# Optimization experiments

Measured on AMD Instinct MI355X. Metric: run time of the kernel, lower is better.

The kernel has to match this reference:

```python
import jax, jax.numpy as jnp
import numpy as np

B, SQ, SC, D = 16, 1024, 1024, 768
H = 2 * D  # 1536, fc width
NCLS = 2


def setup_inputs() -> dict:
    key = jax.random.key(0)
    ks = jax.random.split(key, 8)
    q = jax.random.normal(ks[0], (B, SQ, D), jnp.float32)
    c = jax.random.normal(ks[1], (B, SC, D), jnp.float32)
    mask_q = jax.random.randint(ks[2], (B, SQ), 0, 2).astype(jnp.int32)
    mask_c = jax.random.randint(ks[3], (B, SC), 0, 2).astype(jnp.int32)
    labels = jax.random.randint(ks[4], (B,), 0, NCLS)
    # torch nn.Linear convention: weight [out, in], y = x @ W.T + b
    W1 = jax.random.normal(ks[5], (H, H), jnp.float32) * 0.02
    b1 = jnp.zeros((H,), jnp.float32)
    W2 = jax.random.normal(ks[6], (NCLS, H), jnp.float32) * 0.02
    b2 = jnp.zeros((NCLS,), jnp.float32)
    return dict(q=q, c=c, mask_q=mask_q, mask_c=mask_c, labels=labels,
                W1=W1, b1=b1, W2=W2, b2=b2)


def reference(q, c, mask_q, mask_c, labels, W1, b1, W2, b2):
    # masked QK^T score matrix: [B, SQ, SC]
    s = jnp.einsum('bik,bjk->bij', q, c)
    s = s * mask_q[:, :, None].astype(s.dtype) * mask_c[:, None, :].astype(s.dtype)
    s = jnp.where(s == 0.0, -jnp.inf, s)  # x[x == 0.0] = -inf
    p = jnp.nan_to_num(jax.nn.softmax(s, axis=2))   # softmax over context axis
    pp = jnp.nan_to_num(jax.nn.softmax(s, axis=1))  # softmax over question axis
    a = jnp.einsum('bjk,bij->bk', c, p)   # weighted combine into context feats
    bb = jnp.einsum('bik,bij->bk', q, pp)  # weighted combine into question feats
    x = jnp.concatenate([a, bb], axis=1)  # [B, 1536]
    x = jnp.tanh(x @ W1.T + b1)           # fc1 + tanh (dropout = identity in eval)
    logits = x @ W2.T + b2                # fc2
    logp = jax.nn.log_softmax(logits, axis=1)  # LogSoftmax(dim=1)
    # NLLLoss (mean reduction)
    loss = -jnp.mean(jnp.take_along_axis(logp, labels[:, None], axis=1))
    return (loss, logp)
```

## Files before the change

### kernel.cpp

```cpp
#include <hip/hip_runtime.h>
#include <math.h>

#define B_   16
#define SQ_  1024
#define SC_  1024
#define D_   768
#define H_   1536
#define BK   32
#define LDK  40

typedef __attribute__((ext_vector_type(4))) float f32x4;
typedef __attribute__((ext_vector_type(8))) short bf16x8;

__device__ __forceinline__ unsigned cvtpk(float x, float y) {
  unsigned r;
  asm("v_cvt_pk_bf16_f32 %0, %1, %2" : "=v"(r) : "v"(x), "v"(y));
  return r;
}

__device__ __forceinline__ void split4(float4 v, uint2& hi, uint2& lo) {
  unsigned h01 = cvtpk(v.x, v.y);
  unsigned h23 = cvtpk(v.z, v.w);
  float h0 = __uint_as_float(h01 << 16);
  float h1 = __uint_as_float(h01 & 0xFFFF0000u);
  float h2 = __uint_as_float(h23 << 16);
  float h3 = __uint_as_float(h23 & 0xFFFF0000u);
  hi = make_uint2(h01, h23);
  lo = make_uint2(cvtpk(v.x - h0, v.y - h1), cvtpk(v.z - h2, v.w - h3));
}

__device__ __forceinline__ double exp_pos(float s) {
  float t = s * 1.4426950408889634f;
  float n = floorf(t);
  float p = exp2f(t - n);
  long long e = (long long)n;
  double scale = __longlong_as_double((unsigned long long)(e + 1023LL) << 52);
  return (double)p * scale;
}

__global__ __launch_bounds__(256) void compact_kernel(
    const int* __restrict__ mask_q, const int* __restrict__ mask_c,
    int* __restrict__ idx_q, int* __restrict__ idx_c, int* __restrict__ cnt,
    float* __restrict__ zeroA, int lenA, float* __restrict__ zeroB, int lenB)
{
  int which = blockIdx.x & 1;
  int b     = blockIdx.x >> 1;
  const int* m = (which ? mask_c : mask_q) + b * 1024;
  int* idx     = (which ? idx_c : idx_q) + b * 1024;

  int t = threadIdx.x;
  int gid = blockIdx.x * 256 + t;
  for (int i = gid; i < lenA; i += 32 * 256) zeroA[i] = 0.f;
  for (int i = gid; i < lenB; i += 32 * 256) zeroB[i] = 0.f;

  __shared__ int tsum[256];
  int v[4], s = 0;
#pragma unroll
  for (int e = 0; e < 4; ++e) { v[e] = (m[t * 4 + e] != 0) ? 1 : 0; s += v[e]; }
  tsum[t] = s;
  __syncthreads();
  for (int off = 1; off < 256; off <<= 1) {
    int add = (t >= off) ? tsum[t - off] : 0;
    __syncthreads();
    tsum[t] += add;
    __syncthreads();
  }
  int pos = tsum[t] - s;
#pragma unroll
  for (int e = 0; e < 4; ++e) {
    if (v[e]) idx[pos++] = t * 4 + e;
  }
  if (t == 255) cnt[b * 2 + which] = tsum[255];
}

__global__ __launch_bounds__(256) void gemm_mfma_kernel(
    const float* __restrict__ q, const float* __restrict__ c,
    const int* __restrict__ idx_q, const int* __restrict__ idx_c,
    const int* __restrict__ cnt,
    float* __restrict__ S, double* __restrict__ R, double* __restrict__ C)
{
  __shared__ unsigned short Ah[2][64][LDK];
  __shared__ unsigned short Al[2][64][LDK];
  __shared__ unsigned short Bh[2][64][LDK];
  __shared__ unsigned short Bl[2][64][LDK];

  const int bb = blockIdx.z;
  const int i0 = blockIdx.y * 64;
  const int j0 = blockIdx.x * 64;
  const int nq = cnt[2 * bb], nc = cnt[2 * bb + 1];
  if (i0 >= nq || j0 >= nc) return;

  const int t    = threadIdx.x;
  const int lane = t & 63;
  const int w    = t >> 6;

  const int srow = t >> 2;
  const int kc   = (t & 3) * 4;
  const int fr   = lane & 15;
  const int fq   = lane >> 4;
  const int kg   = fq * 8;

  const int rq = idx_q[bb * 1024 + min(i0 + srow, nq - 1)];
  const int rc = idx_c[bb * 1024 + min(j0 + srow, nc - 1)];
  const float* qrowP = q + ((size_t)bb * SQ_ + rq) * D_;
  const float* crowP = c + ((size_t)bb * SC_ + rc) * D_;

  f32x4 acc[4] = {};

  float4 av0 = *(const float4*)(qrowP + kc);
  float4 av1 = *(const float4*)(qrowP + kc + 16);
  float4 bv0 = *(const float4*)(crowP + kc);
  float4 bv1 = *(const float4*)(crowP + kc + 16);
  {
    uint2 hi, lo;
    split4(av0, hi, lo); *(uint2*)&Ah[0][srow][kc]      = hi; *(uint2*)&Al[0][srow][kc]      = lo;
    split4(av1, hi, lo); *(uint2*)&Ah[0][srow][kc + 16] = hi; *(uint2*)&Al[0][srow][kc + 16] = lo;
    split4(bv0, hi, lo); *(uint2*)&Bh[0][srow][kc]      = hi; *(uint2*)&Bl[0][srow][kc]      = lo;
    split4(bv1, hi, lo); *(uint2*)&Bh[0][srow][kc + 16] = hi; *(uint2*)&Bl[0][srow][kc + 16] = lo;
  }
  __syncthreads();

  int cur = 0;
  for (int k0 = 0; k0 < D_; k0 += BK) {
    const int next = k0 + BK;
    const bool has_next = (next < D_);
    if (has_next) {
      av0 = *(const float4*)(qrowP + next + kc);
      av1 = *(const float4*)(qrowP + next + kc + 16);
      bv0 = *(const float4*)(crowP + next + kc);
      bv1 = *(const float4*)(crowP + next + kc + 16);
    }

    bf16x8 b_h = *reinterpret_cast<const bf16x8*>(&Bh[cur][w * 16 + fr][kg]);
    bf16x8 b_l = *reinterpret_cast<const bf16x8*>(&Bl[cur][w * 16 + fr][kg]);
#pragma unroll
    for (int m = 0; m < 4; ++m) {
      bf16x8 a_h = *reinterpret_cast<const bf16x8*>(&Ah[cur][m * 16 + fr][kg]);
      bf16x8 a_l = *reinterpret_cast<const bf16x8*>(&Al[cur][m * 16 + fr][kg]);
      acc[m] = __builtin_amdgcn_mfma_f32_16x16x32_bf16(a_h, b_h, acc[m], 0, 0, 0);
      acc[m] = __builtin_amdgcn_mfma_f32_16x16x32_bf16(a_h, b_l, acc[m], 0, 0, 0);
      acc[m] = __builtin_amdgcn_mfma_f32_16x16x32_bf16(a_l, b_h, acc[m], 0, 0, 0);
    }

    if (has_next) {
      int nxt = cur ^ 1;
      uint2 hi, lo;
      split4(av0, hi, lo); *(uint2*)&Ah[nxt][srow][kc]      = hi; *(uint2*)&Al[nxt][srow][kc]      = lo;
      split4(av1, hi, lo); *(uint2*)&Ah[nxt][srow][kc + 16] = hi; *(uint2*)&Al[nxt][srow][kc + 16] = lo;
      split4(bv0, hi, lo); *(uint2*)&Bh[nxt][srow][kc]      = hi; *(uint2*)&Bl[nxt][srow][kc]      = lo;
      split4(bv1, hi, lo); *(uint2*)&Bh[nxt][srow][kc + 16] = hi; *(uint2*)&Bl[nxt][srow][kc + 16] = lo;
    }
    __syncthreads();
    cur ^= 1;
  }

  const int col = j0 + w * 16 + fr;
  const bool cok = (col < nc);
  double rowPart[4][4];
  double colSum = 0.0;
#pragma unroll
  for (int m = 0; m < 4; ++m) {
    const int rbase = i0 + m * 16 + fq * 4;
    float* Sp = S + ((size_t)bb * SQ_ + rbase) * SC_ + col;
#pragma unroll
    for (int rr = 0; rr < 4; ++rr) {
      float v = acc[m][rr];
      bool valid = ((rbase + rr) < nq) && cok && (v != 0.f);
      Sp[(size_t)rr * SC_] = valid ? v : -INFINITY;
      double e = valid ? exp_pos(v) : 0.0;
      colSum += e;
      rowPart[m][rr] = e;
    }
  }
#pragma unroll
  for (int m = 0; m < 4; ++m)
#pragma unroll
    for (int rr = 0; rr < 4; ++rr) {
      double x = rowPart[m][rr];
      x += __shfl_xor(x, 1); x += __shfl_xor(x, 2);
      x += __shfl_xor(x, 4); x += __shfl_xor(x, 8);
      rowPart[m][rr] = x;
    }
  if (fr == 0) {
#pragma unroll
    for (int m = 0; m < 4; ++m)
#pragma unroll
      for (int rr = 0; rr < 4; ++rr) {
        double x = rowPart[m][rr];
        if (x != 0.0) atomicAdd(&R[bb * SQ_ + i0 + m * 16 + fq * 4 + rr], x);
      }
  }
  {
    double x = colSum;
    x += __shfl_xor(x, 16); x += __shfl_xor(x, 32);
    if (fq == 0 && cok && x != 0.0) atomicAdd(&C[bb * SC_ + col], x);
  }
}

__global__ __launch_bounds__(1024) void pass2_kernel(
    const float* __restrict__ S, const int* __restrict__ cnt,
    const double* __restrict__ R, const double* __restrict__ C,
    float* __restrict__ cp, float* __restrict__ rpp)
{
  __shared__ float lnR_lds[SQ_];
  __shared__ float red[16][64];

  int b  = blockIdx.y;
  int j0 = blockIdx.x * 64;
  int nq_pad = (cnt[2 * b] + 63) & ~63;
  int nc_pad = (cnt[2 * b + 1] + 63) & ~63;
  if (j0 >= nc_pad) return;
  int t = threadIdx.x;

  if (t < nq_pad) {
    double Ri = R[b * SQ_ + t];
    lnR_lds[t] = (Ri > 0.0) ? (float)log(Ri) : INFINITY;
  }
  __syncthreads();

  int lane = t & 63, wv = t >> 6;
  int j = j0 + lane;
  double Cj = C[b * SC_ + j];
  float lnCj = (Cj > 0.0) ? (float)log(Cj) : INFINITY;

  int chunk = nq_pad >> 4;
  int i0 = wv * chunk;
  const float* Sb = S + ((size_t)b * SQ_ + i0) * SC_ + j;

  float cpAcc = 0.f;
  for (int ii = 0; ii < chunk; ++ii) {
    int i = i0 + ii;
    float v = Sb[(size_t)ii * SC_];
    cpAcc += __expf(v - lnR_lds[i]);
    float e2 = __expf(v - lnCj);
#pragma unroll
    for (int o = 32; o; o >>= 1) e2 += __shfl_xor(e2, o);
    if (lane == 0) atomicAdd(&rpp[b * SQ_ + i], e2);
  }

  red[wv][lane] = cpAcc;
  __syncthreads();
  if (t < 64) {
    float s = 0.f;
#pragma unroll
    for (int k = 0; k < 16; ++k) s += red[k][t];
    cp[b * SC_ + j0 + t] = s;
  }
}

__global__ __launch_bounds__(256) void combine_kernel(
    const float* __restrict__ q, const float* __restrict__ c,
    const int* __restrict__ idx_q, const int* __restrict__ idx_c,
    const int* __restrict__ cnt,
    const float* __restrict__ cp, const float* __restrict__ rpp,
    float* __restrict__ X)
{
  int jc = blockIdx.x;
  int op = blockIdx.y;
  int b  = blockIdx.z;
  int t  = threadIdx.x;

  int n = op ? cnt[2 * b] : cnt[2 * b + 1];
  const float* src = op ? (q + (size_t)b * SQ_ * D_) : (c + (size_t)b * SC_ * D_);
  const float* wv  = op ? (rpp + b * SQ_) : (cp + b * SC_);
  const int*   idx = (op ? idx_q : idx_c) + b * 1024;

  float a0 = 0.f, a1 = 0.f, a2 = 0.f;
  int je = min(jc * 32 + 32, n);
  for (int j = jc * 32; j < je; ++j) {
    float wj = wv[j];
    const float* r = src + (size_t)idx[j] * D_;
    a0 += wj * r[t];
    a1 += wj * r[t + 256];
    a2 += wj * r[t + 512];
  }
  float* xp = X + (size_t)b * H_ + op * D_;
  atomicAdd(&xp[t], a0);
  atomicAdd(&xp[t + 256], a1);
  atomicAdd(&xp[t + 512], a2);
}

__global__ __launch_bounds__(256) void fc1_kernel(
    const float* __restrict__ X, const float* __restrict__ W1,
    const float* __restrict__ b1, float* __restrict__ Y)
{
  int w = threadIdx.x >> 6, lane = threadIdx.x & 63;
  int h = blockIdx.x * 4 + w;
  const float4* wr = (const float4*)(W1 + (size_t)h * H_);
  float4 wv[6];
#pragma unroll
  for (int it = 0; it < 6; ++it) wv[it] = wr[it * 64 + lane];
  float bias = b1[h];

  for (int b = 0; b < B_; ++b) {
    const float4* x = (const float4*)(X + (size_t)b * H_);
    float accv = 0.f;
#pragma unroll
    for (int it = 0; it < 6; ++it) {
      float4 xv = x[it * 64 + lane];
      accv += xv.x * wv[it].x + xv.y * wv[it].y + xv.z * wv[it].z + xv.w * wv[it].w;
    }
#pragma unroll
    for (int o = 32; o; o >>= 1) accv += __shfl_xor(accv, o);
    if (lane == 0) Y[(size_t)b * H_ + h] = tanhf(accv + bias);
  }
}

__global__ __launch_bounds__(64) void fc2_loss_kernel(
    const float* __restrict__ Y, const float* __restrict__ W2,
    const float* __restrict__ b2, const int* __restrict__ labels,
    float* __restrict__ out)
{
  __shared__ float logp_s[B_][2];
  int t = threadIdx.x;
  if (t < 2 * B_) {
    int b = t >> 1, n = t & 1;
    const float* y = Y + (size_t)b * H_;
    const float* w = W2 + (size_t)n * H_;
    float accv = b2[n];
    for (int k = 0; k < H_; ++k) accv += y[k] * w[k];
    logp_s[b][n] = accv;
  }
  __syncthreads();
  if (t < B_) {
    float l0 = logp_s[t][0], l1 = logp_s[t][1];
    float m = fmaxf(l0, l1);
    float lse = m + logf(expf(l0 - m) + expf(l1 - m));
    logp_s[t][0] = l0 - lse;
    logp_s[t][1] = l1 - lse;
  }
  __syncthreads();
  if (t < 2 * B_) out[1 + t] = logp_s[t >> 1][t & 1];
  if (t == 0) {
    float loss = 0.f;
    for (int b = 0; b < B_; ++b) loss -= logp_s[b][labels[b]];
    out[0] = loss / (float)B_;
  }
}

extern "C" void kernel_launch(void* const* d_in, const int* in_sizes, int n_in,
                              void* d_out, int out_size, void* d_ws, size_t ws_size,
                              hipStream_t stream) {
  const float* q      = (const float*)d_in[0];
  const float* c      = (const float*)d_in[1];
  const int*   mask_q = (const int*)d_in[2];
  const int*   mask_c = (const int*)d_in[3];
  const int*   labels = (const int*)d_in[4];
  const float* W1     = (const float*)d_in[5];
  const float* b1     = (const float*)d_in[6];
  const float* W2     = (const float*)d_in[7];
  const float* b2     = (const float*)d_in[8];
  float* out = (float*)d_out;

  float*  ws    = (float*)d_ws;
  float*  S     = ws;
  double* R     = (double*)(ws + (size_t)B_ * SQ_ * SC_);
  double* C     = R + B_ * SQ_;
  float*  cp    = (float*)(C + B_ * SC_);
  float*  rpp   = cp + B_ * SC_;
  int*    cnt   = (int*)(rpp + B_ * SQ_);
  int*    idx_q = cnt + 2 * B_;
  int*    idx_c = idx_q + B_ * SQ_;
  float*  X     = (float*)(idx_c + B_ * SC_);
  float*  Y     = X + B_ * H_;
  float*  zeroA = (float*)R;
  const int lenA = 2 * B_ * SQ_ * 2 + 2 * B_ * SC_;
  const int lenB = B_ * H_;

  compact_kernel<<<2 * B_, 256, 0, stream>>>(mask_q, mask_c, idx_q, idx_c, cnt,
                                             zeroA, lenA, X, lenB);

  dim3 g1(SC_ / 64, SQ_ / 64, B_);
  gemm_mfma_kernel<<<g1, 256, 0, stream>>>(q, c, idx_q, idx_c, cnt, S, R, C);

  pass2_kernel<<<dim3(SC_ / 64, B_), 1024, 0, stream>>>(S, cnt, R, C, cp, rpp);

  combine_kernel<<<dim3(32, 2, B_), 256, 0, stream>>>(q, c, idx_q, idx_c, cnt,
                                                      cp, rpp, X);
  fc1_kernel<<<H_ / 4, 256, 0, stream>>>(X, W1, b1, Y);
  fc2_loss_kernel<<<1, 64, 0, stream>>>(Y, W2, b2, labels, out);
}
```

Measured before the change: 180.5 us.

## Restructure score GEMM into a single-wave 64x64 tile with swizzled LDS

The score GEMM now runs one 64-thread wave per block, and that wave computes the whole 64x64 tile with a 4x4 array of MFMA accumulators instead of four waves each owning a 16-column strip. The hi and lo bf16 halves are packed into one XOR-swizzled LDS row per matrix, and the double buffer and block barriers are dropped. The next K slice is prefetched into registers during the MFMAs. The aim is to reuse each LDS fragment across four MFMA tiles, cut redundant A-fragment loads and avoid LDS bank conflicts. The cost is much higher register pressure and far fewer waves per CU for hiding global-load latency.

```diff
diff --git a/kernel.cpp b/kernel.cpp
--- a/kernel.cpp
+++ b/kernel.cpp
@@ -6,8 +6,6 @@
 #define SC_  1024
 #define D_   768
 #define H_   1536
-#define BK   32
-#define LDK  40
 
 typedef __attribute__((ext_vector_type(4))) float f32x4;
 typedef __attribute__((ext_vector_type(8))) short bf16x8;
@@ -73,16 +71,14 @@
   if (t == 255) cnt[b * 2 + which] = tsum[255];
 }
 
-__global__ __launch_bounds__(256) void gemm_mfma_kernel(
+__global__ __launch_bounds__(64) void gemm_mfma_kernel(
     const float* __restrict__ q, const float* __restrict__ c,
     const int* __restrict__ idx_q, const int* __restrict__ idx_c,
     const int* __restrict__ cnt,
     float* __restrict__ S, double* __restrict__ R, double* __restrict__ C)
 {
-  __shared__ unsigned short Ah[2][64][LDK];
-  __shared__ unsigned short Al[2][64][LDK];
-  __shared__ unsigned short Bh[2][64][LDK];
-  __shared__ unsigned short Bl[2][64][LDK];
+  __shared__ unsigned short Ahl[64 * 64];
+  __shared__ unsigned short Bhl[64 * 64];
 
   const int bb = blockIdx.z;
   const int i0 = blockIdx.y * 64;
@@ -90,86 +86,98 @@
   const int nq = cnt[2 * bb], nc = cnt[2 * bb + 1];
   if (i0 >= nq || j0 >= nc) return;
 
-  const int t    = threadIdx.x;
-  const int lane = t & 63;
-  const int w    = t >> 6;
-
-  const int srow = t >> 2;
-  const int kc   = (t & 3) * 4;
-  const int fr   = lane & 15;
-  const int fq   = lane >> 4;
-  const int kg   = fq * 8;
-
-  const int rq = idx_q[bb * 1024 + min(i0 + srow, nq - 1)];
-  const int rc = idx_c[bb * 1024 + min(j0 + srow, nc - 1)];
-  const float* qrowP = q + ((size_t)bb * SQ_ + rq) * D_;
-  const float* crowP = c + ((size_t)bb * SC_ + rc) * D_;
-
-  f32x4 acc[4] = {};
-
-  float4 av0 = *(const float4*)(qrowP + kc);
-  float4 av1 = *(const float4*)(qrowP + kc + 16);
-  float4 bv0 = *(const float4*)(crowP + kc);
-  float4 bv1 = *(const float4*)(crowP + kc + 16);
-  {
-    uint2 hi, lo;
-    split4(av0, hi, lo); *(uint2*)&Ah[0][srow][kc]      = hi; *(uint2*)&Al[0][srow][kc]      = lo;
-    split4(av1, hi, lo); *(uint2*)&Ah[0][srow][kc + 16] = hi; *(uint2*)&Al[0][srow][kc + 16] = lo;
-    split4(bv0, hi, lo); *(uint2*)&Bh[0][srow][kc]      = hi; *(uint2*)&Bl[0][srow][kc]      = lo;
-    split4(bv1, hi, lo); *(uint2*)&Bh[0][srow][kc + 16] = hi; *(uint2*)&Bl[0][srow][kc + 16] = lo;
-  }
-  __syncthreads();
-
-  int cur = 0;
-  for (int k0 = 0; k0 < D_; k0 += BK) {
-    const int next = k0 + BK;
-    const bool has_next = (next < D_);
-    if (has_next) {
-      av0 = *(const float4*)(qrowP + next + kc);
-      av1 = *(const float4*)(qrowP + next + kc + 16);
-      bv0 = *(const float4*)(crowP + next + kc);
-      bv1 = *(const float4*)(crowP + next + kc + 16);
-    }
-
-    bf16x8 b_h = *reinterpret_cast<const bf16x8*>(&Bh[cur][w * 16 + fr][kg]);
-    bf16x8 b_l = *reinterpret_cast<const bf16x8*>(&Bl[cur][w * 16 + fr][kg]);
+  const int l   = threadIdx.x;
+  const int fr  = l & 15;
+  const int fq  = l >> 4;
+  const int sr8 = l >> 3;
+  const int sc4 = (l & 7) * 4;
+
+  const float* aP[8];
+  const float* bP[8];
+#pragma unroll
+  for (int g = 0; g < 8; ++g) {
+    int ra = idx_q[bb * 1024 + min(i0 + g * 8 + sr8, nq - 1)];
+    int rb = idx_c[bb * 1024 + min(j0 + g * 8 + sr8, nc - 1)];
+    aP[g] = q + ((size_t)bb * SQ_ + ra) * D_ + sc4;
+    bP[g] = c + ((size_t)bb * SC_ + rb) * D_ + sc4;
+  }
+
+  f32x4 acc[4][4] = {};
+
+  float4 av[8], bv[8];
+#pragma unroll
+  for (int g = 0; g < 8; ++g) {
+    av[g] = *(const float4*)(aP[g]);
+    bv[g] = *(const float4*)(bP[g]);
+  }
+
+  for (int k0 = 0; k0 < D_; k0 += 32) {
+#pragma unroll
+    for (int g = 0; g < 8; ++g) {
+      const int row = g * 8 + sr8;
+      const int swz = (row & 7) << 3;
+      uint2 hi, lo;
+      split4(av[g], hi, lo);
+      *(uint2*)&Ahl[row * 64 + (sc4 ^ swz)]        = hi;
+      *(uint2*)&Ahl[row * 64 + ((32 + sc4) ^ swz)] = lo;
+      split4(bv[g], hi, lo);
+      *(uint2*)&Bhl[row * 64 + (sc4 ^ swz)]        = hi;
+      *(uint2*)&Bhl[row * 64 + ((32 + sc4) ^ swz)] = lo;
+    }
+
+    const int nk = k0 + 32;
+    if (nk < D_) {
+#pragma unroll
+      for (int g = 0; g < 8; ++g) {
+        av[g] = *(const float4*)(aP[g] + nk);
+        bv[g] = *(const float4*)(bP[g] + nk);
+      }
+    }
+
+    bf16x8 a_h[4], a_l[4], b_h[4], b_l[4];
 #pragma unroll
     for (int m = 0; m < 4; ++m) {
-      bf16x8 a_h = *reinterpret_cast<const bf16x8*>(&Ah[cur][m * 16 + fr][kg]);
-      bf16x8 a_l = *reinterpret_cast<const bf16x8*>(&Al[cur][m * 16 + fr][kg]);
-      acc[m] = __builtin_amdgcn_mfma_f32_16x16x32_bf16(a_h, b_h, acc[m], 0, 0, 0);
-      acc[m] = __builtin_amdgcn_mfma_f32_16x16x32_bf16(a_h, b_l, acc[m], 0, 0, 0);
-      acc[m] = __builtin_amdgcn_mfma_f32_16x16x32_bf16(a_l, b_h, acc[m], 0, 0, 0);
-    }
-
-    if (has_next) {
-      int nxt = cur ^ 1;
-      uint2 hi, lo;
-      split4(av0, hi, lo); *(uint2*)&Ah[nxt][srow][kc]      = hi; *(uint2*)&Al[nxt][srow][kc]      = lo;
-      split4(av1, hi, lo); *(uint2*)&Ah[nxt][srow][kc + 16] = hi; *(uint2*)&Al[nxt][srow][kc + 16] = lo;
-      split4(bv0, hi, lo); *(uint2*)&Bh[nxt][srow][kc]      = hi; *(uint2*)&Bl[nxt][srow][kc]      = lo;
-      split4(bv1, hi, lo); *(uint2*)&Bh[nxt][srow][kc + 16] = hi; *(uint2*)&Bl[nxt][srow][kc + 16] = lo;
-    }
-    __syncthreads();
-    cur ^= 1;
-  }
-
-  const int col = j0 + w * 16 + fr;
-  const bool cok = (col < nc);
+      const int row = m * 16 + fr;
+      const int swz = (row & 7) << 3;
+      a_h[m] = *(const bf16x8*)&Ahl[row * 64 + ((fq * 8) ^ swz)];
+      a_l[m] = *(const bf16x8*)&Ahl[row * 64 + ((32 + fq * 8) ^ swz)];
+      b_h[m] = *(const bf16x8*)&Bhl[row * 64 + ((fq * 8) ^ swz)];
+      b_l[m] = *(const bf16x8*)&Bhl[row * 64 + ((32 + fq * 8) ^ swz)];
+    }
+#pragma unroll
+    for (int n = 0; n < 4; ++n)
+#pragma unroll
+      for (int m = 0; m < 4; ++m) {
+        acc[m][n] = __builtin_amdgcn_mfma_f32_16x16x32_bf16(a_h[m], b_h[n], acc[m][n], 0, 0, 0);
+        acc[m][n] = __builtin_amdgcn_mfma_f32_16x16x32_bf16(a_h[m], b_l[n], acc[m][n], 0, 0, 0);
+        acc[m][n] = __builtin_amdgcn_mfma_f32_16x16x32_bf16(a_l[m], b_h[n], acc[m][n], 0, 0, 0);
+      }
+  }
+
   double rowPart[4][4];
-  double colSum = 0.0;
+#pragma unroll
+  for (int m = 0; m < 4; ++m)
+#pragma unroll
+    for (int rr = 0; rr < 4; ++rr) rowPart[m][rr] = 0.0;
+  double colSum[4] = {0.0, 0.0, 0.0, 0.0};
+
 #pragma unroll
   for (int m = 0; m < 4; ++m) {
     const int rbase = i0 + m * 16 + fq * 4;
-    float* Sp = S + ((size_t)bb * SQ_ + rbase) * SC_ + col;
-#pragma unroll
-    for (int rr = 0; rr < 4; ++rr) {
-      float v = acc[m][rr];
-      bool valid = ((rbase + rr) < nq) && cok && (v != 0.f);
-      Sp[(size_t)rr * SC_] = valid ? v : -INFINITY;
-      double e = valid ? exp_pos(v) : 0.0;
-      colSum += e;
-      rowPart[m][rr] = e;
+#pragma unroll
+    for (int n = 0; n < 4; ++n) {
+      const int col = j0 + n * 16 + fr;
+      const bool cok = (col < nc);
+      float* Sp = S + ((size_t)bb * SQ_ + rbase) * SC_ + col;
+#pragma unroll
+      for (int rr = 0; rr < 4; ++rr) {
+        float v = acc[m][n][rr];
+        bool valid = ((rbase + rr) < nq) && cok && (v != 0.f);
+        Sp[(size_t)rr * SC_] = valid ? v : -INFINITY;
+        double e = valid ? exp_pos(v) : 0.0;
+        colSum[n] += e;
+        rowPart[m][rr] += e;
+      }
     }
   }
 #pragma unroll
@@ -190,10 +198,14 @@
         if (x != 0.0) atomicAdd(&R[bb * SQ_ + i0 + m * 16 + fq * 4 + rr], x);
       }
   }
-  {
-    double x = colSum;
+#pragma unroll
+  for (int n = 0; n < 4; ++n) {
+    double x = colSum[n];
     x += __shfl_xor(x, 16); x += __shfl_xor(x, 32);
-    if (fq == 0 && cok && x != 0.0) atomicAdd(&C[bb * SC_ + col], x);
+    if (fq == 0 && x != 0.0) {
+      int col = j0 + n * 16 + fr;
+      if (col < nc) atomicAdd(&C[bb * SC_ + col], x);
+    }
   }
 }
 
@@ -371,7 +383,7 @@
                                              zeroA, lenA, X, lenB);
 
   dim3 g1(SC_ / 64, SQ_ / 64, B_);
-  gemm_mfma_kernel<<<g1, 256, 0, stream>>>(q, c, idx_q, idx_c, cnt, S, R, C);
+  gemm_mfma_kernel<<<g1, 64, 0, stream>>>(q, c, idx_q, idx_c, cnt, S, R, C);
 
   pass2_kernel<<<dim3(SC_ / 64, B_), 1024, 0, stream>>>(S, cnt, R, C, cp, rpp);
 
```

Result: slower. 202.5 us (+12.2%).
